# Kernel optimization log

Measured on AMD Instinct MI355X. Metric: run time of the kernel, lower is better.

Reference implementation:

```python
import jax, jax.numpy as jnp
import numpy as np

B, T, C = 8, 2048, 1024
NEG = -1e30  # stand-in for -inf in the stable-softmax running max


def setup_inputs() -> dict:
    key = jax.random.key(0)
    ks = jax.random.split(key, 5)
    x = jax.random.normal(ks[0], (B, T, C), dtype=jnp.float32)
    scales = jnp.arange(C, dtype=jnp.float32) / C  # matches init_weight()
    Wk = jax.random.normal(ks[1], (C, C), dtype=jnp.float32) * 0.02
    Wv = jax.random.normal(ks[2], (C, C), dtype=jnp.float32) * 0.02
    Wr = jax.random.normal(ks[3], (C, C), dtype=jnp.float32) * 0.02
    Wo = jax.random.normal(ks[4], (C, C), dtype=jnp.float32) * 0.02
    return {
        'x': x,
        'w': scales, 'u': scales,
        'mix_k': scales, 'mix_v': scales, 'mix_r': scales,
        'Wk': Wk, 'Wv': Wv, 'Wr': Wr, 'Wo': Wo,
    }


def wkv(w, u, k, v):
    # Numerically-stable RWKV WKV recurrence. k, v: [B, T, C]; w, u: [C]
    w_exp = -jnp.exp(w)  # per-channel log-decay (negative)
    p0 = jnp.zeros(k.shape[::2], k.dtype)      # [B, C] numerator state
    q0 = jnp.zeros(k.shape[::2], k.dtype)      # [B, C] denominator state
    o0 = jnp.full(k.shape[::2], NEG, k.dtype)  # [B, C] running max (log-space)

    def step(carry, kv_t):
        p, q, o = carry
        k_t, v_t = kv_t  # each [B, C]
        uk = u + k_t
        no = jnp.maximum(o, uk)
        A = jnp.exp(o - no)
        Bc = jnp.exp(uk - no)
        out = (A * p + Bc * v_t) / (A * q + Bc)
        wo = w_exp + o
        no2 = jnp.maximum(wo, k_t)
        A2 = jnp.exp(wo - no2)
        B2 = jnp.exp(k_t - no2)
        return (A2 * p + B2 * v_t, A2 * q + B2, no2), out

    kT = jnp.swapaxes(k, 0, 1)  # [T, B, C]
    vT = jnp.swapaxes(v, 0, 1)
    _, outs = jax.lax.scan(step, (p0, q0, o0), (kT, vT))
    return jnp.swapaxes(outs, 0, 1)  # [B, T, C]


def reference(x, w, u, mix_k, mix_v, mix_r, Wk, Wv, Wr, Wo):
    # time_shift: ZeroPad2d((0,0,1,-1)) => shift sequence right by one, zero-pad front
    x_prev = jnp.pad(x, ((0, 0), (1, 0), (0, 0)))[:, :-1]
    # torch.lerp(start=x_prev, end=x, weight=mix)
    xk = x_prev + mix_k * (x - x_prev)
    xv = x_prev + mix_v * (x - x_prev)
    xr = x_prev + mix_r * (x - x_prev)
    k = jnp.einsum('btc,dc->btd', xk, Wk)
    v = jnp.einsum('btc,dc->btd', xv, Wv)
    sr = jax.nn.sigmoid(jnp.einsum('btc,dc->btd', xr, Wr))
    rwkv = sr * wkv(w, u, k, v)
    return jnp.einsum('btc,dc->btd', rwkv, Wo)
```

## Files before the change

### kernel.cpp

```cpp
#include <hip/hip_runtime.h>
#include <hip/hip_bf16.h>
#include <stdint.h>

#define Bb   8
#define Tt   2048
#define Cdim 1024
#define BT   16384

#define NC   32
#define LCH  64
#define CSUB 32

typedef __attribute__((ext_vector_type(4))) float f32x4;
typedef __attribute__((ext_vector_type(8))) short bf16x8;

__device__ inline short f2bs(float f) {
    union { __hip_bfloat16 h; short s; } u;
    u.h = __float2bfloat16(f);
    return u.s;
}
__device__ inline float bs2f(short s) {
    union { short s; __hip_bfloat16 h; } u;
    u.s = s;
    return __bfloat162float(u.h);
}

#define GLOAD_LDS16(g, l) __builtin_amdgcn_global_load_lds( \
    (const __attribute__((address_space(1))) void*)(g),     \
    (__attribute__((address_space(3))) void*)(l), 16, 0, 0)

#define SBAR()      __builtin_amdgcn_s_barrier()
#define WAIT_LGKM0  asm volatile("s_waitcnt lgkmcnt(0)" ::: "memory")

__global__ __launch_bounds__(256) void prep_x(
    const float* __restrict__ x,
    const float* __restrict__ mk,
    const float* __restrict__ mv,
    const float* __restrict__ mr,
    short* __restrict__ xmix)
{
    int idx = blockIdx.x * 256 + threadIdx.x;
    int c8  = idx & (Cdim / 8 - 1);
    int m   = idx >> 7;
    int c0  = c8 << 3;
    int t   = m & (Tt - 1);

    float xs[8], ps[8];
    const float4* xp = (const float4*)(x + (size_t)m * Cdim + c0);
    float4 xa = xp[0], xb = xp[1];
    xs[0]=xa.x; xs[1]=xa.y; xs[2]=xa.z; xs[3]=xa.w;
    xs[4]=xb.x; xs[5]=xb.y; xs[6]=xb.z; xs[7]=xb.w;
    if (t != 0) {
        const float4* pp = (const float4*)(x + (size_t)(m - 1) * Cdim + c0);
        float4 pa = pp[0], pb = pp[1];
        ps[0]=pa.x; ps[1]=pa.y; ps[2]=pa.z; ps[3]=pa.w;
        ps[4]=pb.x; ps[5]=pb.y; ps[6]=pb.z; ps[7]=pb.w;
    } else {
        #pragma unroll
        for (int j = 0; j < 8; ++j) ps[j] = 0.f;
    }

    const float* mixes[3] = {mk, mv, mr};
    #pragma unroll
    for (int z = 0; z < 3; ++z) {
        const float4* mp = (const float4*)(mixes[z] + c0);
        float4 ma = mp[0], mb = mp[1];
        float mm[8];
        mm[0]=ma.x; mm[1]=ma.y; mm[2]=ma.z; mm[3]=ma.w;
        mm[4]=mb.x; mm[5]=mb.y; mm[6]=mb.z; mm[7]=mb.w;
        bf16x8 o;
        #pragma unroll
        for (int j = 0; j < 8; ++j)
            o[j] = f2bs(ps[j] + mm[j] * (xs[j] - ps[j]));
        *(bf16x8*)(xmix + (size_t)z * BT * Cdim + (size_t)m * Cdim + c0) = o;
    }
}

__global__ __launch_bounds__(256) void prep_w(
    const float* __restrict__ Wk, const float* __restrict__ Wv,
    const float* __restrict__ Wr, const float* __restrict__ Wo,
    short* __restrict__ wbf)
{
    int idx = blockIdx.x * 256 + threadIdx.x;
    int z   = idx >> 17;
    int r   = idx & (Cdim * Cdim / 8 - 1);
    const float* src = (z == 0) ? Wk : (z == 1) ? Wv : (z == 2) ? Wr : Wo;
    const float4* sp = (const float4*)(src + (size_t)r * 8);
    float4 a = sp[0], b = sp[1];
    float v[8] = {a.x, a.y, a.z, a.w, b.x, b.y, b.z, b.w};
    bf16x8 o;
    #pragma unroll
    for (int j = 0; j < 8; ++j) o[j] = f2bs(v[j]);
    *(bf16x8*)(wbf + (size_t)z * Cdim * Cdim + (size_t)r * 8) = o;
}

template<int MODE>
__global__ __launch_bounds__(512, 2) void gemm256(
    const short* __restrict__ A,
    const short* __restrict__ Bm,
    void* __restrict__ Cout,
    int M, int N, int K)
{
    __shared__ __align__(16) short lds[65536];

    const int tid  = threadIdx.x;
    const int lane = tid & 63;
    const int wv   = tid >> 6;
    const int wm   = wv >> 2, wn = wv & 3;
    const int m0 = blockIdx.y * 256;
    const int n0 = blockIdx.x * 256;
    const int NT = K >> 5;

    f32x4 acc[8][4] = {};

    int a_off[8], b_off[4];
    #pragma unroll
    for (int i = 0; i < 8; ++i) {
        int r = wm * 128 + i * 16 + (lane & 15);
        a_off[i] = r * 32 + ((((lane >> 4) ^ ((r >> 1) & 3))) << 3);
    }
    #pragma unroll
    for (int j = 0; j < 4; ++j) {
        int r = wn * 64 + j * 16 + (lane & 15);
        b_off[j] = r * 32 + ((((lane >> 4) ^ ((r >> 1) & 3))) << 3);
    }

    auto STAGE = [&](int tt, int p) {
        int row = ((p & 1) << 7) + (tid >> 2);
        int cc  = (tid & 3) ^ ((row >> 1) & 3);
        const short* g = ((p < 2) ? (A + (size_t)(m0 + row) * K)
                                  : (Bm + (size_t)(n0 + row) * K))
                         + (tt << 5) + (cc << 3);
        short* l = lds + ((tt & 3) << 14) + ((p < 2) ? 0 : 8192)
                       + ((p & 1) << 12) + tid * 8;
        GLOAD_LDS16(g, l);
    };

    #pragma unroll
    for (int p = 0; p < 4; ++p) STAGE(0, p);
    #pragma unroll
    for (int p = 0; p < 4; ++p) STAGE(1, p);
    asm volatile("s_waitcnt vmcnt(4)" ::: "memory");
    SBAR();

    #pragma unroll 1
    for (int kt = 0; kt < NT; ++kt) {
        const short* la = lds + ((kt & 3) << 14);
        const short* lb = la + 8192;
        const bool st = (kt + 2) < NT;

        bf16x8 afr[4], bfr[4];
        #pragma unroll
        for (int i = 0; i < 4; ++i) afr[i] = *(const bf16x8*)(la + a_off[i]);
        #pragma unroll
        for (int j = 0; j < 4; ++j) bfr[j] = *(const bf16x8*)(lb + b_off[j]);
        if (st) { STAGE(kt + 2, 0); STAGE(kt + 2, 1); }
        SBAR();
        WAIT_LGKM0;
        __builtin_amdgcn_sched_barrier(0);
        __builtin_amdgcn_s_setprio(1);
        #pragma unroll
        for (int i = 0; i < 4; ++i)
            #pragma unroll
            for (int j = 0; j < 4; ++j)
                acc[i][j] = __builtin_amdgcn_mfma_f32_16x16x32_bf16(
                    afr[i], bfr[j], acc[i][j], 0, 0, 0);
        __builtin_amdgcn_s_setprio(0);
        SBAR();

        bf16x8 af2[4];
        #pragma unroll
        for (int i = 0; i < 4; ++i) af2[i] = *(const bf16x8*)(la + a_off[i + 4]);
        if (st) { STAGE(kt + 2, 2); STAGE(kt + 2, 3); }
        SBAR();
        WAIT_LGKM0;
        __builtin_amdgcn_sched_barrier(0);
        __builtin_amdgcn_s_setprio(1);
        #pragma unroll
        for (int i = 0; i < 4; ++i)
            #pragma unroll
            for (int j = 0; j < 4; ++j)
                acc[i + 4][j] = __builtin_amdgcn_mfma_f32_16x16x32_bf16(
                    af2[i], bfr[j], acc[i + 4][j], 0, 0, 0);
        __builtin_amdgcn_s_setprio(0);
        if (kt < NT - 2) { asm volatile("s_waitcnt vmcnt(4)" ::: "memory"); }
        else             { asm volatile("s_waitcnt vmcnt(0)" ::: "memory"); }
        SBAR();
    }

    int col0 = n0 + wn * 64 + (lane & 15);
    int row0 = m0 + wm * 128 + ((lane >> 4) << 2);
    #pragma unroll
    for (int i = 0; i < 8; ++i) {
        #pragma unroll
        for (int j = 0; j < 4; ++j) {
            #pragma unroll
            for (int r = 0; r < 4; ++r) {
                int row = row0 + i * 16 + r;
                int cc  = col0 + j * 16;
                float vvv = acc[i][j][r];
                if (MODE == 0)
                    ((float*)Cout)[(size_t)row * N + cc] = vvv;
                else if (MODE == 1)
                    ((short*)Cout)[(size_t)row * N + cc] = f2bs(vvv);
                else
                    ((short*)Cout)[(size_t)row * N + cc] =
                        f2bs(1.f / (1.f + __expf(-vvv)));
            }
        }
    }
}

__global__ __launch_bounds__(1024) void wkv_chunked(
    const short* __restrict__ kb, const short* __restrict__ vb,
    const short* __restrict__ srb,
    const float* __restrict__ w, const float* __restrict__ u,
    short* __restrict__ rwkv)
{
    __shared__ float sp[NC][CSUB];
    __shared__ float sq[NC][CSUB];
    __shared__ float so[NC][CSUB];

    int tid = threadIdx.x;
    int cl  = tid & (CSUB - 1);
    int ch  = tid >> 5;
    int b   = blockIdx.x >> 5;
    int cg  = blockIdx.x & 31;
    int c   = cg * CSUB + cl;

    float wexp = -__expf(w[c]);
    float uu   = u[c];
    size_t coff = (size_t)b * Tt * Cdim + (size_t)(ch * LCH) * Cdim + c;

    float p = 0.f, q = 0.f, o = -1e30f;
    #pragma unroll 8
    for (int t = 0; t < LCH; ++t) {
        size_t off = coff + (size_t)t * Cdim;
        float kt = bs2f(kb[off]);
        float vt = bs2f(vb[off]);
        float wo  = wexp + o;
        float no  = fmaxf(wo, kt);
        float A   = __expf(wo - no);
        float B2  = __expf(kt - no);
        p = A * p + B2 * vt;
        q = A * q + B2;
        o = no;
    }
    sp[ch][cl] = p; sq[ch][cl] = q; so[ch][cl] = o;
    __syncthreads();

    if (tid < CSUB) {
        float Ld = wexp * (float)LCH;
        float cp = 0.f, cq = 0.f, co = -1e30f;
        for (int j = 0; j < NC; ++j) {
            float lp = sp[j][tid], lq = sq[j][tid], lo = so[j][tid];
            sp[j][tid] = cp; sq[j][tid] = cq; so[j][tid] = co;
            float od = co + Ld;
            float no = fmaxf(od, lo);
            float A  = __expf(od - no);
            float B2 = __expf(lo - no);
            cp = A * cp + B2 * lp;
            cq = A * cq + B2 * lq;
            co = no;
        }
    }
    __syncthreads();

    p = sp[ch][cl]; q = sq[ch][cl]; o = so[ch][cl];
    #pragma unroll 4
    for (int t = 0; t < LCH; ++t) {
        size_t off = coff + (size_t)t * Cdim;
        float kt = bs2f(kb[off]);
        float vt = bs2f(vb[off]);
        float sr = bs2f(srb[off]);

        float uk  = uu + kt;
        float no  = fmaxf(o, uk);
        float Aa  = __expf(o - no);
        float Bc  = __expf(uk - no);
        float out = (Aa * p + Bc * vt) / (Aa * q + Bc);

        float wo  = wexp + o;
        float no2 = fmaxf(wo, kt);
        float A2  = __expf(wo - no2);
        float B2  = __expf(kt - no2);
        p = A2 * p + B2 * vt;
        q = A2 * q + B2;
        o = no2;

        rwkv[off] = f2bs(sr * out);
    }
}

extern "C" void kernel_launch(void* const* d_in, const int* in_sizes, int n_in,
                              void* d_out, int out_size, void* d_ws, size_t ws_size,
                              hipStream_t stream)
{
    const float* x    = (const float*)d_in[0];
    const float* w    = (const float*)d_in[1];
    const float* u    = (const float*)d_in[2];
    const float* mixk = (const float*)d_in[3];
    const float* mixv = (const float*)d_in[4];
    const float* mixr = (const float*)d_in[5];
    const float* Wk   = (const float*)d_in[6];
    const float* Wv   = (const float*)d_in[7];
    const float* Wr   = (const float*)d_in[8];
    const float* Wo   = (const float*)d_in[9];

    const size_t SLAB = (size_t)BT * Cdim;
    char* ws = (char*)d_ws;
    short* xmix = (short*)ws;
    short* wbf  = (short*)(ws + 3 * SLAB * 2);
    short* rbuf = (short*)(ws + 3 * SLAB * 2 + (size_t)4 * Cdim * Cdim * 2);
    short* rwkv = (short*)ws;
    short* kbuf = (short*)d_out;
    short* vbuf = kbuf + SLAB;

    prep_x<<<BT * Cdim / 8 / 256, 256, 0, stream>>>(x, mixk, mixv, mixr, xmix);
    prep_w<<<4 * Cdim * Cdim / 8 / 256, 256, 0, stream>>>(Wk, Wv, Wr, Wo, wbf);

    dim3 g2(Cdim / 256, BT / 256);
    gemm256<1><<<g2, 512, 0, stream>>>(xmix,            wbf,                   kbuf, BT, Cdim, Cdim);
    gemm256<1><<<g2, 512, 0, stream>>>(xmix + SLAB,     wbf + Cdim * Cdim,     vbuf, BT, Cdim, Cdim);
    gemm256<2><<<g2, 512, 0, stream>>>(xmix + 2 * SLAB, wbf + 2 * Cdim * Cdim, rbuf, BT, Cdim, Cdim);

    wkv_chunked<<<Bb * (Cdim / CSUB), 1024, 0, stream>>>(kbuf, vbuf, rbuf, w, u, rwkv);

    gemm256<0><<<g2, 512, 0, stream>>>(rwkv, wbf + 3 * Cdim * Cdim, (float*)d_out, BT, Cdim, Cdim);
}
```

Measured before the change: 264.9 us.

## Fuse K/V/R GEMMs into one launch, deepen prefetch, remap WKV chunks

The three projection GEMMs become a single launch that picks which projection to run from the workgroup index, using an XCD-aware remap of that index to improve L2 locality. The GEMM prefetch depth goes from 2 to 3 stages within the existing 4-buffer LDS ring, with the vmcnt waits adjusted to match. The WKV kernel switches to shorter chunks over fewer channels per block (64 chunks of 32 steps, 16 channels), giving more blocks and a longer serial carry scan, and its loops are unrolled further. The aim is to cut launch tail effects and hide global-load latency, at the cost of more complex index math and a 3-deep pipeline sharing a 4-slot buffer.

```diff
diff --git a/kernel.cpp b/kernel.cpp
--- a/kernel.cpp
+++ b/kernel.cpp
@@ -6,10 +6,11 @@
 #define Tt   2048
 #define Cdim 1024
 #define BT   16384
-
-#define NC   32
-#define LCH  64
-#define CSUB 32
+#define SLAB ((size_t)BT * Cdim)
+
+#define NC   64
+#define LCH  32
+#define CSUB 16
 
 typedef __attribute__((ext_vector_type(4))) float f32x4;
 typedef __attribute__((ext_vector_type(8))) short bf16x8;
@@ -72,7 +73,7 @@
         #pragma unroll
         for (int j = 0; j < 8; ++j)
             o[j] = f2bs(ps[j] + mm[j] * (xs[j] - ps[j]));
-        *(bf16x8*)(xmix + (size_t)z * BT * Cdim + (size_t)m * Cdim + c0) = o;
+        *(bf16x8*)(xmix + (size_t)z * SLAB + (size_t)m * Cdim + c0) = o;
     }
 }
 
@@ -94,12 +95,11 @@
     *(bf16x8*)(wbf + (size_t)z * Cdim * Cdim + (size_t)r * 8) = o;
 }
 
-template<int MODE>
+template<int FUSED>
 __global__ __launch_bounds__(512, 2) void gemm256(
-    const short* __restrict__ A,
-    const short* __restrict__ Bm,
-    void* __restrict__ Cout,
-    int M, int N, int K)
+    const short* __restrict__ Abase,
+    const short* __restrict__ Wbase,
+    void* __restrict__ o0, void* __restrict__ o1, void* __restrict__ o2)
 {
     __shared__ __align__(16) short lds[65536];
 
@@ -107,9 +107,20 @@
     const int lane = tid & 63;
     const int wv   = tid >> 6;
     const int wm   = wv >> 2, wn = wv & 3;
-    const int m0 = blockIdx.y * 256;
-    const int n0 = blockIdx.x * 256;
-    const int NT = K >> 5;
+    const int NT   = Cdim / 32;
+
+    int orig = blockIdx.y * gridDim.x + blockIdx.x;
+    int nwg  = gridDim.x * gridDim.y;
+    int wid  = (orig & 7) * (nwg >> 3) + (orig >> 3);
+
+    int yt, nt, z;
+    if (FUSED) { yt = wid / 12; int xt = wid % 12; z = xt >> 2; nt = xt & 3; }
+    else       { yt = wid >> 2; nt = wid & 3; z = 0; }
+
+    const short* A  = Abase + (size_t)z * SLAB;
+    const short* Bm = Wbase + (size_t)z * Cdim * Cdim;
+    const int m0 = yt * 256;
+    const int n0 = nt * 256;
 
     f32x4 acc[8][4] = {};
 
@@ -128,8 +139,8 @@
     auto STAGE = [&](int tt, int p) {
         int row = ((p & 1) << 7) + (tid >> 2);
         int cc  = (tid & 3) ^ ((row >> 1) & 3);
-        const short* g = ((p < 2) ? (A + (size_t)(m0 + row) * K)
-                                  : (Bm + (size_t)(n0 + row) * K))
+        const short* g = ((p < 2) ? (A + (size_t)(m0 + row) * Cdim)
+                                  : (Bm + (size_t)(n0 + row) * Cdim))
                          + (tt << 5) + (cc << 3);
         short* l = lds + ((tt & 3) << 14) + ((p < 2) ? 0 : 8192)
                        + ((p & 1) << 12) + tid * 8;
@@ -140,21 +151,23 @@
     for (int p = 0; p < 4; ++p) STAGE(0, p);
     #pragma unroll
     for (int p = 0; p < 4; ++p) STAGE(1, p);
-    asm volatile("s_waitcnt vmcnt(4)" ::: "memory");
+    #pragma unroll
+    for (int p = 0; p < 4; ++p) STAGE(2, p);
+    asm volatile("s_waitcnt vmcnt(8)" ::: "memory");
     SBAR();
 
     #pragma unroll 1
     for (int kt = 0; kt < NT; ++kt) {
         const short* la = lds + ((kt & 3) << 14);
         const short* lb = la + 8192;
-        const bool st = (kt + 2) < NT;
+        const bool st = (kt + 3) < NT;
 
         bf16x8 afr[4], bfr[4];
         #pragma unroll
         for (int i = 0; i < 4; ++i) afr[i] = *(const bf16x8*)(la + a_off[i]);
         #pragma unroll
         for (int j = 0; j < 4; ++j) bfr[j] = *(const bf16x8*)(lb + b_off[j]);
-        if (st) { STAGE(kt + 2, 0); STAGE(kt + 2, 1); }
+        if (st) { STAGE(kt + 3, 0); STAGE(kt + 3, 1); }
         SBAR();
         WAIT_LGKM0;
         __builtin_amdgcn_sched_barrier(0);
@@ -171,7 +184,7 @@
         bf16x8 af2[4];
         #pragma unroll
         for (int i = 0; i < 4; ++i) af2[i] = *(const bf16x8*)(la + a_off[i + 4]);
-        if (st) { STAGE(kt + 2, 2); STAGE(kt + 2, 3); }
+        if (st) { STAGE(kt + 3, 2); STAGE(kt + 3, 3); }
         SBAR();
         WAIT_LGKM0;
         __builtin_amdgcn_sched_barrier(0);
@@ -183,13 +196,16 @@
                 acc[i + 4][j] = __builtin_amdgcn_mfma_f32_16x16x32_bf16(
                     af2[i], bfr[j], acc[i + 4][j], 0, 0, 0);
         __builtin_amdgcn_s_setprio(0);
-        if (kt < NT - 2) { asm volatile("s_waitcnt vmcnt(4)" ::: "memory"); }
-        else             { asm volatile("s_waitcnt vmcnt(0)" ::: "memory"); }
+        if      (kt <  NT - 3) { asm volatile("s_waitcnt vmcnt(8)" ::: "memory"); }
+        else if (kt == NT - 3) { asm volatile("s_waitcnt vmcnt(4)" ::: "memory"); }
+        else if (kt == NT - 2) { asm volatile("s_waitcnt vmcnt(0)" ::: "memory"); }
         SBAR();
     }
 
     int col0 = n0 + wn * 64 + (lane & 15);
     int row0 = m0 + wm * 128 + ((lane >> 4) << 2);
+    short* outb = 0;
+    if (FUSED) outb = (short*)((z == 0) ? o0 : (z == 1) ? o1 : o2);
     #pragma unroll
     for (int i = 0; i < 8; ++i) {
         #pragma unroll
@@ -199,13 +215,12 @@
                 int row = row0 + i * 16 + r;
                 int cc  = col0 + j * 16;
                 float vvv = acc[i][j][r];
-                if (MODE == 0)
-                    ((float*)Cout)[(size_t)row * N + cc] = vvv;
-                else if (MODE == 1)
-                    ((short*)Cout)[(size_t)row * N + cc] = f2bs(vvv);
-                else
-                    ((short*)Cout)[(size_t)row * N + cc] =
-                        f2bs(1.f / (1.f + __expf(-vvv)));
+                if (FUSED) {
+                    if (z == 2) vvv = 1.f / (1.f + __expf(-vvv));
+                    outb[(size_t)row * Cdim + cc] = f2bs(vvv);
+                } else {
+                    ((float*)o0)[(size_t)row * Cdim + cc] = vvv;
+                }
             }
         }
     }
@@ -223,9 +238,9 @@
 
     int tid = threadIdx.x;
     int cl  = tid & (CSUB - 1);
-    int ch  = tid >> 5;
-    int b   = blockIdx.x >> 5;
-    int cg  = blockIdx.x & 31;
+    int ch  = tid >> 4;
+    int b   = blockIdx.x >> 6;
+    int cg  = blockIdx.x & 63;
     int c   = cg * CSUB + cl;
 
     float wexp = -__expf(w[c]);
@@ -252,6 +267,7 @@
     if (tid < CSUB) {
         float Ld = wexp * (float)LCH;
         float cp = 0.f, cq = 0.f, co = -1e30f;
+        #pragma unroll 8
         for (int j = 0; j < NC; ++j) {
             float lp = sp[j][tid], lq = sq[j][tid], lo = so[j][tid];
             sp[j][tid] = cp; sq[j][tid] = cq; so[j][tid] = co;
@@ -267,7 +283,7 @@
     __syncthreads();
 
     p = sp[ch][cl]; q = sq[ch][cl]; o = so[ch][cl];
-    #pragma unroll 4
+    #pragma unroll 8
     for (int t = 0; t < LCH; ++t) {
         size_t off = coff + (size_t)t * Cdim;
         float kt = bs2f(kb[off]);
@@ -307,7 +323,6 @@
     const float* Wr   = (const float*)d_in[8];
     const float* Wo   = (const float*)d_in[9];
 
-    const size_t SLAB = (size_t)BT * Cdim;
     char* ws = (char*)d_ws;
     short* xmix = (short*)ws;
     short* wbf  = (short*)(ws + 3 * SLAB * 2);
@@ -319,12 +334,12 @@
     prep_x<<<BT * Cdim / 8 / 256, 256, 0, stream>>>(x, mixk, mixv, mixr, xmix);
     prep_w<<<4 * Cdim * Cdim / 8 / 256, 256, 0, stream>>>(Wk, Wv, Wr, Wo, wbf);
 
-    dim3 g2(Cdim / 256, BT / 256);
-    gemm256<1><<<g2, 512, 0, stream>>>(xmix,            wbf,                   kbuf, BT, Cdim, Cdim);
-    gemm256<1><<<g2, 512, 0, stream>>>(xmix + SLAB,     wbf + Cdim * Cdim,     vbuf, BT, Cdim, Cdim);
-    gemm256<2><<<g2, 512, 0, stream>>>(xmix + 2 * SLAB, wbf + 2 * Cdim * Cdim, rbuf, BT, Cdim, Cdim);
+    dim3 gf(12, BT / 256);
+    gemm256<1><<<gf, 512, 0, stream>>>(xmix, wbf, kbuf, vbuf, rbuf);
 
     wkv_chunked<<<Bb * (Cdim / CSUB), 1024, 0, stream>>>(kbuf, vbuf, rbuf, w, u, rwkv);
 
-    gemm256<0><<<g2, 512, 0, stream>>>(rwkv, wbf + 3 * Cdim * Cdim, (float*)d_out, BT, Cdim, Cdim);
-}
+    dim3 go(Cdim / 256, BT / 256);
+    gemm256<0><<<go, 512, 0, stream>>>(rwkv, wbf + 3 * (size_t)Cdim * Cdim,
+                                       (float*)d_out, nullptr, nullptr);
+}
```

Result: slower. 313.0 us (+18.2%).
